# Kernel tuning notes

Measured on AMD Instinct MI355X. Metric: run time of the kernel, lower is better.

Reference implementation:

```python
import jax, jax.numpy as jnp
import numpy as np

B, T, C = 2, 2048, 2048
NH, NKV, HD = 16, 4, 128
GATE_CH = 12
WINDOW = 1024


def apply_rotary_emb(x, cos, sin):
    # x: (B,T,H,HD); cos/sin: (1,T,1,HD//2)
    d = x.shape[3] // 2
    x1, x2 = x[..., :d], x[..., d:]
    return jnp.concatenate([x1 * cos + x2 * sin, -x1 * sin + x2 * cos], axis=3)


def rms_norm(x):
    return x * jax.lax.rsqrt(jnp.mean(jnp.square(x), axis=-1, keepdims=True) + 1e-06)


def setup_inputs() -> dict:
    key = jax.random.key(0)
    ks = jax.random.split(key, 7)
    # realistic RoPE tables
    theta = 10000.0 ** (-jnp.arange(HD // 2, dtype=jnp.float32) / (HD // 2))
    ang = jnp.arange(T, dtype=jnp.float32)[:, None] * theta[None, :]
    cos = jnp.cos(ang)[None, :, None, :]
    sin = jnp.sin(ang)[None, :, None, :]
    return {
        "x": jax.random.normal(ks[0], (B, T, C), jnp.float32),
        "ve": jax.random.normal(ks[1], (B, T, NKV * HD), jnp.float32),
        "cos": cos,
        "sin": sin,
        "Wq": 0.02 * jax.random.normal(ks[2], (NH * HD, C), jnp.float32),
        "Wk": 0.02 * jax.random.normal(ks[3], (NKV * HD, C), jnp.float32),
        "Wv": 0.02 * jax.random.normal(ks[4], (NKV * HD, C), jnp.float32),
        "Wproj": 0.02 * jax.random.normal(ks[5], (C, C), jnp.float32),
        "Wgate": 0.02 * jax.random.normal(ks[6], (NKV, GATE_CH), jnp.float32),
        "window_size": WINDOW,
    }


def reference(x, ve, cos, sin, Wq, Wk, Wv, Wproj, Wgate, window_size):
    B_, T_, C_ = x.shape
    q = (x @ Wq.T).reshape(B_, T_, NH, HD)
    k = (x @ Wk.T).reshape(B_, T_, NKV, HD)
    v = (x @ Wv.T).reshape(B_, T_, NKV, HD)
    # value-embedding gate-add
    gate = 3.0 * jax.nn.sigmoid(x[..., :GATE_CH] @ Wgate.T)  # (B,T,NKV)
    v = v + gate[..., None] * ve.reshape(B_, T_, NKV, HD)
    # RoPE + QK RMSNorm + scale
    q = rms_norm(apply_rotary_emb(q, cos, sin)) * 1.2
    k = rms_norm(apply_rotary_emb(k, cos, sin)) * 1.2
    # GQA head-repeat
    rep = NH // NKV
    k = jnp.repeat(k, rep, axis=2)
    v = jnp.repeat(v, rep, axis=2)
    # sliding-window causal bias (window_size > 0 branch)
    r = jnp.arange(T_)
    mask = (r[None, :] <= r[:, None]) & (r[:, None] - r[None, :] <= window_size)
    bias = jnp.where(mask, 0.0, jnp.finfo(x.dtype).min)  # (T,T)
    scores = jnp.einsum("bthd,bshd->bhts", q, k) * (1.0 / np.sqrt(HD).astype(np.float32))
    scores = scores + bias[None, None, :, :]
    w = jax.nn.softmax(scores, axis=-1)
    y = jnp.einsum("bhts,bshd->bthd", w, v).reshape(B_, T_, -1)
    return y @ Wproj.T
```

## Files before the change

kernel.cpp:

```cpp
#include <hip/hip_runtime.h>
#include <hip/hip_bf16.h>

#define BB   2
#define TT   2048
#define CC   2048
#define NHq  16
#define NKVq 4
#define HDq  128
#define ROWS (BB*TT)
#define NQKV (NHq*HDq + 2*NKVq*HDq)

using bf16 = __hip_bfloat16;
using short8  = __attribute__((ext_vector_type(8))) short;
using short4v = __attribute__((ext_vector_type(4))) short;
using f32x4   = __attribute__((ext_vector_type(4))) float;

#define MFMA16(a,b,c) __builtin_amdgcn_mfma_f32_16x16x32_bf16((a),(b),(c),0,0,0)

__device__ __forceinline__ void gll16(const bf16* g, void* l) {
    __builtin_amdgcn_global_load_lds((const __attribute__((address_space(1))) void*)g,
                                     (__attribute__((address_space(3))) void*)l,
                                     16, 0, 0);
}

__global__ void cast_all(const float* __restrict__ x,  const float* __restrict__ wq,
                         const float* __restrict__ wk, const float* __restrict__ wv,
                         const float* __restrict__ wp, bf16* __restrict__ dst) {
    long e = ((long)blockIdx.x * 256 + threadIdx.x) * 4;
    const float* src; long off;
    if (e < 8388608L)       { src = x;  off = e; }
    else if (e < 12582912L) { src = wq; off = e - 8388608L; }
    else if (e < 13631488L) { src = wk; off = e - 12582912L; }
    else if (e < 14680064L) { src = wv; off = e - 13631488L; }
    else                    { src = wp; off = e - 14680064L; }
    float4 v = *reinterpret_cast<const float4*>(src + off);
    ushort4 o;
    o.x = __bfloat16_as_ushort(__float2bfloat16(v.x));
    o.y = __bfloat16_as_ushort(__float2bfloat16(v.y));
    o.z = __bfloat16_as_ushort(__float2bfloat16(v.z));
    o.w = __bfloat16_as_ushort(__float2bfloat16(v.w));
    *reinterpret_cast<ushort4*>(dst + e) = o;
}

template<int OUT_F32>
__global__ __launch_bounds__(256) void gemm_bt(const bf16* __restrict__ A,
                                               const bf16* __restrict__ B,
                                               void* __restrict__ Cp,
                                               int M, int N, int K) {
    const int bm = blockIdx.x * 128;
    const int bn = blockIdx.y * 128;
    const int tid = threadIdx.x;
    const int lane = tid & 63;
    const int w = tid >> 6;
    const int wr = w >> 1, wc = w & 1;

    __shared__ __align__(16) bf16 As[128 * 64];
    __shared__ __align__(16) bf16 Bs[128 * 64];

    f32x4 acc[4][4];
#pragma unroll
    for (int i = 0; i < 4; ++i)
#pragma unroll
        for (int j = 0; j < 4; ++j) acc[i][j] = f32x4{0.f, 0.f, 0.f, 0.f};

    const int srow = tid >> 3;
    const int sch  = tid & 7;

    const int fr = lane & 15;
    const int kq = lane >> 4;

    for (int k0 = 0; k0 < K; k0 += 64) {
        __syncthreads();
#pragma unroll
        for (int i = 0; i < 4; ++i) {
            int row = i * 32 + srow;
            int c = sch ^ (row & 7);
            gll16(&A[(size_t)(bm + row) * K + k0 + c * 8], (char*)As + i * 4096 + tid * 16);
            gll16(&B[(size_t)(bn + row) * K + k0 + c * 8], (char*)Bs + i * 4096 + tid * 16);
        }
        __syncthreads();

#pragma unroll
        for (int kk = 0; kk < 2; ++kk) {
            short8 af[4], bfr[4];
#pragma unroll
            for (int m = 0; m < 4; ++m) {
                int r = wr * 64 + m * 16 + fr;
                af[m] = *reinterpret_cast<const short8*>(
                    (const char*)As + r * 128 + (((kk * 4 + kq) ^ (r & 7)) * 16));
            }
#pragma unroll
            for (int n = 0; n < 4; ++n) {
                int r = wc * 64 + n * 16 + fr;
                bfr[n] = *reinterpret_cast<const short8*>(
                    (const char*)Bs + r * 128 + (((kk * 4 + kq) ^ (r & 7)) * 16));
            }
            __builtin_amdgcn_s_setprio(1);
#pragma unroll
            for (int m = 0; m < 4; ++m)
#pragma unroll
                for (int n = 0; n < 4; ++n)
                    acc[m][n] = MFMA16(af[m], bfr[n], acc[m][n]);
            __builtin_amdgcn_s_setprio(0);
        }
    }

    const int cr = (lane >> 4) * 4;
    const int cc = lane & 15;
#pragma unroll
    for (int m = 0; m < 4; ++m)
#pragma unroll
        for (int n = 0; n < 4; ++n) {
            int row = bm + wr * 64 + m * 16 + cr;
            int col = bn + wc * 64 + n * 16 + cc;
#pragma unroll
            for (int j = 0; j < 4; ++j) {
                float v = acc[m][n][j];
                if (OUT_F32) ((float*)Cp)[(size_t)(row + j) * N + col] = v;
                else         ((bf16*)Cp)[(size_t)(row + j) * N + col] = __float2bfloat16(v);
            }
        }
}

__global__ __launch_bounds__(256) void postproc(const float* __restrict__ x,
                                                const float* __restrict__ ve,
                                                const float* __restrict__ cosb,
                                                const float* __restrict__ sinb,
                                                const float* __restrict__ Wgate,
                                                bf16* __restrict__ qkv) {
    const int row = blockIdx.x;
    const int t = row & (TT - 1);
    const int tid = threadIdx.x;
    __shared__ float gate_s[NKVq];
    if (tid < NKVq) {
        float g = 0.f;
#pragma unroll
        for (int c = 0; c < 12; ++c) g += x[(size_t)row * CC + c] * Wgate[tid * 12 + c];
        gate_s[tid] = 3.0f / (1.0f + __expf(-g));
    }
    __syncthreads();

    bf16* qkvr = qkv + (size_t)row * NQKV;

#pragma unroll
    for (int i = 0; i < 2; ++i) {
        int idx = tid + i * 256;
        float v = __bfloat162float(qkvr[2560 + idx]);
        v += gate_s[idx >> 7] * ve[(size_t)row * 512 + idx];
        qkvr[2560 + idx] = __float2bfloat16(v);
    }

    const int lane = tid & 63;
    const int w = tid >> 6;
    const float cv = cosb[(size_t)t * 64 + lane];
    const float sv = sinb[(size_t)t * 64 + lane];
    for (int hh = w; hh < NHq + NKVq; hh += 4) {
        int off = (hh < NHq) ? hh * HDq : 2048 + (hh - NHq) * HDq;
        float x1 = __bfloat162float(qkvr[off + lane]);
        float x2 = __bfloat162float(qkvr[off + 64 + lane]);
        float r1 =  x1 * cv + x2 * sv;
        float r2 = -x1 * sv + x2 * cv;
        float ss = r1 * r1 + r2 * r2;
#pragma unroll
        for (int m = 1; m < 64; m <<= 1) ss += __shfl_xor(ss, m);
        float sc = rsqrtf(ss * (1.0f / 128.0f) + 1e-6f) * 1.2f;
        qkvr[off + lane]      = __float2bfloat16(r1 * sc);
        qkvr[off + 64 + lane] = __float2bfloat16(r2 * sc);
    }
}

__global__ __launch_bounds__(256, 2) void attn_mfma(const bf16* __restrict__ qkv,
                                                    bf16* __restrict__ y,
                                                    const int* __restrict__ winp) {
    const int bid = blockIdx.x;
    const int group = bid >> 8, idx = bid & 255;
    const int bh = idx >> 3, jj = idx & 7;
    const int qt = group ? jj : (15 - jj);
    const int h = bh & 15, b = bh >> 4;
    const int t0 = qt * 128;
    const int kvh = h >> 2;
    const int tid = threadIdx.x;
    const int lane = tid & 63;
    const int w = tid >> 6;
    const int window = winp[0];

    __shared__ __align__(16) bf16 Ks[2][64 * 128];
    __shared__ __align__(16) bf16 Vt[2][128 * 64];
    __shared__ __align__(16) bf16 Ps[4][32 * 64];

    const int fr = lane & 15;
    const int kq = (lane >> 4) * 8;
    const int hi = lane >> 4;
    const float scl2 = 0.08838834764831845f * 1.4426950408889634f;
    const float CAP = 24.0f;

    short8 qf[2][4];
#pragma unroll
    for (int mi = 0; mi < 2; ++mi) {
        const bf16* qp = qkv + ((size_t)(b * TT) + t0 + w * 32 + mi * 16 + fr) * NQKV + h * HDq;
#pragma unroll
        for (int c = 0; c < 4; ++c) {
            short8 v = *reinterpret_cast<const short8*>(&qp[c * 32 + kq]);
#pragma unroll
            for (int e = 0; e < 8; ++e) {
                float f = __bfloat162float(__ushort_as_bfloat16((ushort)v[e])) * scl2;
                v[e] = (short)__bfloat16_as_ushort(__float2bfloat16(f));
            }
            qf[mi][c] = v;
        }
    }

    f32x4 acc[2][8];
#pragma unroll
    for (int mi = 0; mi < 2; ++mi)
#pragma unroll
        for (int n = 0; n < 8; ++n) acc[mi][n] = f32x4{0.f, 0.f, 0.f, 0.f};
    float lrow[2][4];
#pragma unroll
    for (int mi = 0; mi < 2; ++mi)
#pragma unroll
        for (int j = 0; j < 4; ++j) lrow[mi][j] = 0.f;

    int s_lo = t0 - window; if (s_lo < 0) s_lo = 0; s_lo &= ~63;
    const int s_end = t0 + 128;

    const bf16* Kg = qkv + (size_t)b * TT * NQKV + 2048 + kvh * HDq;
    const bf16* Vg = Kg + 512;

    const int str = tid >> 4;
    const int sti = tid & 15;
    const int vf  = tid & 15;
    const int vdc = (tid >> 4) * 8;

    short8 vr[4];

#pragma unroll
    for (int p = 0; p < 4; ++p) {
        int row = p * 16 + str;
        int c16 = sti ^ (row & 7);
        gll16(&Kg[(size_t)(s_lo + row) * NQKV + c16 * 8], (char*)Ks[0] + p * 4096 + tid * 16);
    }
#pragma unroll
    for (int i = 0; i < 4; ++i)
        vr[i] = *reinterpret_cast<const short8*>(&Vg[(size_t)(s_lo + 16 * i + vf) * NQKV + vdc]);
#pragma unroll
    for (int j = 0; j < 8; ++j) {
        short4v col;
        col[0] = vr[0][j]; col[1] = vr[1][j]; col[2] = vr[2][j]; col[3] = vr[3][j];
        *reinterpret_cast<short4v*>((char*)Vt[0] + (vdc + j) * 128 + ((8 * vf) ^ (j << 4))) = col;
    }
    __syncthreads();

    int cur = 0;
    for (int sk = s_lo; sk < s_end; sk += 64) {
        const bool hn = (sk + 64 < s_end);

        if (hn) {
#pragma unroll
            for (int p = 0; p < 4; ++p) {
                int row = p * 16 + str;
                int c16 = sti ^ (row & 7);
                gll16(&Kg[(size_t)(sk + 64 + row) * NQKV + c16 * 8],
                      (char*)Ks[cur ^ 1] + p * 4096 + tid * 16);
            }
#pragma unroll
            for (int i = 0; i < 4; ++i)
                vr[i] = *reinterpret_cast<const short8*>(&Vg[(size_t)(sk + 64 + 16 * i + vf) * NQKV + vdc]);
        }

        f32x4 S[2][4];
#pragma unroll
        for (int mi = 0; mi < 2; ++mi)
#pragma unroll
            for (int n = 0; n < 4; ++n) S[mi][n] = f32x4{0.f, 0.f, 0.f, 0.f};
        __builtin_amdgcn_s_setprio(1);
#pragma unroll
        for (int n = 0; n < 4; ++n) {
            int rb = n * 16 + fr;
#pragma unroll
            for (int c = 0; c < 4; ++c) {
                int colb = c * 64 + kq * 2;
                short8 kf = *reinterpret_cast<const short8*>(
                    (const char*)Ks[cur] + rb * 256 + (colb ^ ((rb & 7) << 4)));
                S[0][n] = MFMA16(qf[0][c], kf, S[0][n]);
                S[1][n] = MFMA16(qf[1][c], kf, S[1][n]);
            }
        }
        __builtin_amdgcn_s_setprio(0);

        const int rw0 = t0 + w * 32;
        const bool interior = (sk + 63 <= rw0) && (rw0 + 31 - sk <= window);
#pragma unroll
        for (int mi = 0; mi < 2; ++mi) {
#pragma unroll
            for (int j = 0; j < 4; ++j) {
                const int rl = hi * 4 + j;
                float s0, s1, s2, s3;
                if (interior) {
                    s0 = S[mi][0][j]; s1 = S[mi][1][j];
                    s2 = S[mi][2][j]; s3 = S[mi][3][j];
                } else {
                    const int r = rw0 + mi * 16 + rl;
                    int c0 = sk + fr, c1 = c0 + 16, c2 = c0 + 32, c3 = c0 + 48;
                    s0 = (c0 <= r && r - c0 <= window) ? S[mi][0][j] : -1e30f;
                    s1 = (c1 <= r && r - c1 <= window) ? S[mi][1][j] : -1e30f;
                    s2 = (c2 <= r && r - c2 <= window) ? S[mi][2][j] : -1e30f;
                    s3 = (c3 <= r && r - c3 <= window) ? S[mi][3][j] : -1e30f;
                }
                float p0 = exp2f(s0 - CAP);
                float p1 = exp2f(s1 - CAP);
                float p2 = exp2f(s2 - CAP);
                float p3 = exp2f(s3 - CAP);
                lrow[mi][j] += (p0 + p1) + (p2 + p3);
                short4v pk;
                pk[0] = (short)__bfloat16_as_ushort(__float2bfloat16(p0));
                pk[1] = (short)__bfloat16_as_ushort(__float2bfloat16(p1));
                pk[2] = (short)__bfloat16_as_ushort(__float2bfloat16(p2));
                pk[3] = (short)__bfloat16_as_ushort(__float2bfloat16(p3));
                const int prow = mi * 16 + rl;
                *reinterpret_cast<short4v*>(
                    (char*)Ps + w * 4096 + prow * 128 + ((8 * fr) ^ ((prow & 7) << 4))) = pk;
            }
        }

        if (hn) {
#pragma unroll
            for (int j = 0; j < 8; ++j) {
                short4v col;
                col[0] = vr[0][j]; col[1] = vr[1][j]; col[2] = vr[2][j]; col[3] = vr[3][j];
                *reinterpret_cast<short4v*>((char*)Vt[cur ^ 1] + (vdc + j) * 128 + ((8 * vf) ^ (j << 4))) = col;
            }
        }

        __builtin_amdgcn_s_setprio(1);
#pragma unroll
        for (int c2 = 0; c2 < 2; ++c2) {
            short8 pa0 = *reinterpret_cast<const short8*>(
                (char*)Ps + w * 4096 + fr * 128 + ((c2 * 64 + hi * 16) ^ ((fr & 7) << 4)));
            short8 pa1 = *reinterpret_cast<const short8*>(
                (char*)Ps + w * 4096 + (16 + fr) * 128 + ((c2 * 64 + hi * 16) ^ ((fr & 7) << 4)));
#pragma unroll
            for (int n = 0; n < 8; ++n) {
                short8 vb = *reinterpret_cast<const short8*>(
                    (char*)Vt[cur] + (n * 16 + fr) * 128 + ((c2 * 64 + hi * 16) ^ ((fr & 7) << 4)));
                acc[0][n] = MFMA16(pa0, vb, acc[0][n]);
                acc[1][n] = MFMA16(pa1, vb, acc[1][n]);
            }
        }
        __builtin_amdgcn_s_setprio(0);

        __syncthreads();
        cur ^= 1;
    }

#pragma unroll
    for (int mi = 0; mi < 2; ++mi)
#pragma unroll
        for (int j = 0; j < 4; ++j) {
            float l = lrow[mi][j];
#pragma unroll
            for (int mm = 1; mm < 16; mm <<= 1) l += __shfl_xor(l, mm);
            const int r = t0 + w * 32 + mi * 16 + hi * 4 + j;
            float inv = 1.f / l;
            bf16* yr = y + ((size_t)(b * TT) + r) * CC + h * HDq;
#pragma unroll
            for (int n = 0; n < 8; ++n)
                yr[n * 16 + fr] = __float2bfloat16(acc[mi][n][j] * inv);
        }
}

extern "C" void kernel_launch(void* const* d_in, const int* in_sizes, int n_in,
                              void* d_out, int out_size, void* d_ws, size_t ws_size,
                              hipStream_t stream) {
    const float* x     = (const float*)d_in[0];
    const float* ve    = (const float*)d_in[1];
    const float* cosb  = (const float*)d_in[2];
    const float* sinb  = (const float*)d_in[3];
    const float* Wq    = (const float*)d_in[4];
    const float* Wk    = (const float*)d_in[5];
    const float* Wv    = (const float*)d_in[6];
    const float* Wproj = (const float*)d_in[7];
    const float* Wgate = (const float*)d_in[8];
    const int*   winp  = (const int*)d_in[9];

    bf16* xb     = (bf16*)d_ws;
    bf16* wqkvb  = xb + (size_t)ROWS * CC;
    bf16* wprojb = wqkvb + (size_t)NQKV * CC;
    bf16* qkvb   = wprojb + (size_t)CC * CC;
    bf16* yb     = xb;

    cast_all<<<18432, 256, 0, stream>>>(x, Wq, Wk, Wv, Wproj, xb);

    gemm_bt<0><<<dim3(ROWS / 128, NQKV / 128), 256, 0, stream>>>(xb, wqkvb, qkvb, ROWS, NQKV, CC);

    postproc<<<ROWS, 256, 0, stream>>>(x, ve, cosb, sinb, Wgate, qkvb);

    attn_mfma<<<BB * NHq * (TT / 128), 256, 0, stream>>>(qkvb, yb, winp);

    gemm_bt<1><<<dim3(ROWS / 128, CC / 128), 256, 0, stream>>>(yb, wprojb, d_out, ROWS, CC, CC);
}
```

Baseline: 178.4 us.

## Split attention query tile across 8 waves and specialize K/V loader waves

The attention kernel now runs 512 threads (8 waves) per 128-row query tile, each wave owning 16 query rows instead of 32. That halves the per-wave accumulator and score registers. K staging moves to waves 4-7 and the V transpose to waves 0-3, so each load path is handled by dedicated waves. This aims to raise wave-level parallelism and latency hiding. The cost is that each K/V fragment read from LDS is reused across fewer rows, which means more LDS traffic per MFMA, and the barrier now has to sync twice as many waves.

```diff
diff --git a/kernel.cpp b/kernel.cpp
--- a/kernel.cpp
+++ b/kernel.cpp
@@ -169,7 +169,7 @@
     }
 }
 
-__global__ __launch_bounds__(256, 2) void attn_mfma(const bf16* __restrict__ qkv,
+__global__ __launch_bounds__(512, 2) void attn_mfma(const bf16* __restrict__ qkv,
                                                     bf16* __restrict__ y,
                                                     const int* __restrict__ winp) {
     const int bid = blockIdx.x;
@@ -186,7 +186,7 @@
 
     __shared__ __align__(16) bf16 Ks[2][64 * 128];
     __shared__ __align__(16) bf16 Vt[2][128 * 64];
-    __shared__ __align__(16) bf16 Ps[4][32 * 64];
+    __shared__ __align__(16) bf16 Ps[8][16 * 64];
 
     const int fr = lane & 15;
     const int kq = (lane >> 4) * 8;
@@ -194,10 +194,9 @@
     const float scl2 = 0.08838834764831845f * 1.4426950408889634f;
     const float CAP = 24.0f;
 
-    short8 qf[2][4];
-#pragma unroll
-    for (int mi = 0; mi < 2; ++mi) {
-        const bf16* qp = qkv + ((size_t)(b * TT) + t0 + w * 32 + mi * 16 + fr) * NQKV + h * HDq;
+    short8 qf[4];
+    {
+        const bf16* qp = qkv + ((size_t)(b * TT) + t0 + w * 16 + fr) * NQKV + h * HDq;
 #pragma unroll
         for (int c = 0; c < 4; ++c) {
             short8 v = *reinterpret_cast<const short8*>(&qp[c * 32 + kq]);
@@ -206,20 +205,14 @@
                 float f = __bfloat162float(__ushort_as_bfloat16((ushort)v[e])) * scl2;
                 v[e] = (short)__bfloat16_as_ushort(__float2bfloat16(f));
             }
-            qf[mi][c] = v;
-        }
-    }
-
-    f32x4 acc[2][8];
-#pragma unroll
-    for (int mi = 0; mi < 2; ++mi)
-#pragma unroll
-        for (int n = 0; n < 8; ++n) acc[mi][n] = f32x4{0.f, 0.f, 0.f, 0.f};
-    float lrow[2][4];
-#pragma unroll
-    for (int mi = 0; mi < 2; ++mi)
-#pragma unroll
-        for (int j = 0; j < 4; ++j) lrow[mi][j] = 0.f;
+            qf[c] = v;
+        }
+    }
+
+    f32x4 acc[8];
+#pragma unroll
+    for (int n = 0; n < 8; ++n) acc[n] = f32x4{0.f, 0.f, 0.f, 0.f};
+    float lrow[4] = {0.f, 0.f, 0.f, 0.f};
 
     int s_lo = t0 - window; if (s_lo < 0) s_lo = 0; s_lo &= ~63;
     const int s_end = t0 + 128;
@@ -227,27 +220,32 @@
     const bf16* Kg = qkv + (size_t)b * TT * NQKV + 2048 + kvh * HDq;
     const bf16* Vg = Kg + 512;
 
-    const int str = tid >> 4;
-    const int sti = tid & 15;
+    const bool isv = (w < 4);
     const int vf  = tid & 15;
-    const int vdc = (tid >> 4) * 8;
+    const int vdc = ((tid >> 4) & 15) * 8;
+    const int ktid = tid & 255;
+    const int str = ktid >> 4;
+    const int sti = ktid & 15;
 
     short8 vr[4];
 
-#pragma unroll
-    for (int p = 0; p < 4; ++p) {
-        int row = p * 16 + str;
-        int c16 = sti ^ (row & 7);
-        gll16(&Kg[(size_t)(s_lo + row) * NQKV + c16 * 8], (char*)Ks[0] + p * 4096 + tid * 16);
-    }
-#pragma unroll
-    for (int i = 0; i < 4; ++i)
-        vr[i] = *reinterpret_cast<const short8*>(&Vg[(size_t)(s_lo + 16 * i + vf) * NQKV + vdc]);
-#pragma unroll
-    for (int j = 0; j < 8; ++j) {
-        short4v col;
-        col[0] = vr[0][j]; col[1] = vr[1][j]; col[2] = vr[2][j]; col[3] = vr[3][j];
-        *reinterpret_cast<short4v*>((char*)Vt[0] + (vdc + j) * 128 + ((8 * vf) ^ (j << 4))) = col;
+    if (!isv) {
+#pragma unroll
+        for (int p = 0; p < 4; ++p) {
+            int row = p * 16 + str;
+            int c16 = sti ^ (row & 7);
+            gll16(&Kg[(size_t)(s_lo + row) * NQKV + c16 * 8], (char*)Ks[0] + p * 4096 + ktid * 16);
+        }
+    } else {
+#pragma unroll
+        for (int i = 0; i < 4; ++i)
+            vr[i] = *reinterpret_cast<const short8*>(&Vg[(size_t)(s_lo + 16 * i + vf) * NQKV + vdc]);
+#pragma unroll
+        for (int j = 0; j < 8; ++j) {
+            short4v col;
+            col[0] = vr[0][j]; col[1] = vr[1][j]; col[2] = vr[2][j]; col[3] = vr[3][j];
+            *reinterpret_cast<short4v*>((char*)Vt[0] + (vdc + j) * 128 + ((8 * vf) ^ (j << 4))) = col;
+        }
     }
     __syncthreads();
 
@@ -256,23 +254,24 @@
         const bool hn = (sk + 64 < s_end);
 
         if (hn) {
-#pragma unroll
-            for (int p = 0; p < 4; ++p) {
-                int row = p * 16 + str;
-                int c16 = sti ^ (row & 7);
-                gll16(&Kg[(size_t)(sk + 64 + row) * NQKV + c16 * 8],
-                      (char*)Ks[cur ^ 1] + p * 4096 + tid * 16);
-            }
-#pragma unroll
-            for (int i = 0; i < 4; ++i)
-                vr[i] = *reinterpret_cast<const short8*>(&Vg[(size_t)(sk + 64 + 16 * i + vf) * NQKV + vdc]);
-        }
-
-        f32x4 S[2][4];
-#pragma unroll
-        for (int mi = 0; mi < 2; ++mi)
-#pragma unroll
-            for (int n = 0; n < 4; ++n) S[mi][n] = f32x4{0.f, 0.f, 0.f, 0.f};
+            if (!isv) {
+#pragma unroll
+                for (int p = 0; p < 4; ++p) {
+                    int row = p * 16 + str;
+                    int c16 = sti ^ (row & 7);
+                    gll16(&Kg[(size_t)(sk + 64 + row) * NQKV + c16 * 8],
+                          (char*)Ks[cur ^ 1] + p * 4096 + ktid * 16);
+                }
+            } else {
+#pragma unroll
+                for (int i = 0; i < 4; ++i)
+                    vr[i] = *reinterpret_cast<const short8*>(&Vg[(size_t)(sk + 64 + 16 * i + vf) * NQKV + vdc]);
+            }
+        }
+
+        f32x4 S[4];
+#pragma unroll
+        for (int n = 0; n < 4; ++n) S[n] = f32x4{0.f, 0.f, 0.f, 0.f};
         __builtin_amdgcn_s_setprio(1);
 #pragma unroll
         for (int n = 0; n < 4; ++n) {
@@ -282,48 +281,42 @@
                 int colb = c * 64 + kq * 2;
                 short8 kf = *reinterpret_cast<const short8*>(
                     (const char*)Ks[cur] + rb * 256 + (colb ^ ((rb & 7) << 4)));
-                S[0][n] = MFMA16(qf[0][c], kf, S[0][n]);
-                S[1][n] = MFMA16(qf[1][c], kf, S[1][n]);
+                S[n] = MFMA16(qf[c], kf, S[n]);
             }
         }
         __builtin_amdgcn_s_setprio(0);
 
-        const int rw0 = t0 + w * 32;
-        const bool interior = (sk + 63 <= rw0) && (rw0 + 31 - sk <= window);
-#pragma unroll
-        for (int mi = 0; mi < 2; ++mi) {
-#pragma unroll
-            for (int j = 0; j < 4; ++j) {
-                const int rl = hi * 4 + j;
-                float s0, s1, s2, s3;
-                if (interior) {
-                    s0 = S[mi][0][j]; s1 = S[mi][1][j];
-                    s2 = S[mi][2][j]; s3 = S[mi][3][j];
-                } else {
-                    const int r = rw0 + mi * 16 + rl;
-                    int c0 = sk + fr, c1 = c0 + 16, c2 = c0 + 32, c3 = c0 + 48;
-                    s0 = (c0 <= r && r - c0 <= window) ? S[mi][0][j] : -1e30f;
-                    s1 = (c1 <= r && r - c1 <= window) ? S[mi][1][j] : -1e30f;
-                    s2 = (c2 <= r && r - c2 <= window) ? S[mi][2][j] : -1e30f;
-                    s3 = (c3 <= r && r - c3 <= window) ? S[mi][3][j] : -1e30f;
-                }
-                float p0 = exp2f(s0 - CAP);
-                float p1 = exp2f(s1 - CAP);
-                float p2 = exp2f(s2 - CAP);
-                float p3 = exp2f(s3 - CAP);
-                lrow[mi][j] += (p0 + p1) + (p2 + p3);
-                short4v pk;
-                pk[0] = (short)__bfloat16_as_ushort(__float2bfloat16(p0));
-                pk[1] = (short)__bfloat16_as_ushort(__float2bfloat16(p1));
-                pk[2] = (short)__bfloat16_as_ushort(__float2bfloat16(p2));
-                pk[3] = (short)__bfloat16_as_ushort(__float2bfloat16(p3));
-                const int prow = mi * 16 + rl;
-                *reinterpret_cast<short4v*>(
-                    (char*)Ps + w * 4096 + prow * 128 + ((8 * fr) ^ ((prow & 7) << 4))) = pk;
-            }
-        }
-
-        if (hn) {
+        const int rw0 = t0 + w * 16;
+        const bool interior = (sk + 63 <= rw0) && (rw0 + 15 - sk <= window);
+#pragma unroll
+        for (int j = 0; j < 4; ++j) {
+            const int rl = hi * 4 + j;
+            float s0, s1, s2, s3;
+            if (interior) {
+                s0 = S[0][j]; s1 = S[1][j]; s2 = S[2][j]; s3 = S[3][j];
+            } else {
+                const int r = rw0 + rl;
+                int c0 = sk + fr, c1 = c0 + 16, c2 = c0 + 32, c3 = c0 + 48;
+                s0 = (c0 <= r && r - c0 <= window) ? S[0][j] : -1e30f;
+                s1 = (c1 <= r && r - c1 <= window) ? S[1][j] : -1e30f;
+                s2 = (c2 <= r && r - c2 <= window) ? S[2][j] : -1e30f;
+                s3 = (c3 <= r && r - c3 <= window) ? S[3][j] : -1e30f;
+            }
+            float p0 = exp2f(s0 - CAP);
+            float p1 = exp2f(s1 - CAP);
+            float p2 = exp2f(s2 - CAP);
+            float p3 = exp2f(s3 - CAP);
+            lrow[j] += (p0 + p1) + (p2 + p3);
+            short4v pk;
+            pk[0] = (short)__bfloat16_as_ushort(__float2bfloat16(p0));
+            pk[1] = (short)__bfloat16_as_ushort(__float2bfloat16(p1));
+            pk[2] = (short)__bfloat16_as_ushort(__float2bfloat16(p2));
+            pk[3] = (short)__bfloat16_as_ushort(__float2bfloat16(p3));
+            *reinterpret_cast<short4v*>(
+                (char*)Ps + w * 2048 + rl * 128 + ((8 * fr) ^ ((rl & 7) << 4))) = pk;
+        }
+
+        if (hn && isv) {
 #pragma unroll
             for (int j = 0; j < 8; ++j) {
                 short4v col;
@@ -335,16 +328,13 @@
         __builtin_amdgcn_s_setprio(1);
 #pragma unroll
         for (int c2 = 0; c2 < 2; ++c2) {
-            short8 pa0 = *reinterpret_cast<const short8*>(
-                (char*)Ps + w * 4096 + fr * 128 + ((c2 * 64 + hi * 16) ^ ((fr & 7) << 4)));
-            short8 pa1 = *reinterpret_cast<const short8*>(
-                (char*)Ps + w * 4096 + (16 + fr) * 128 + ((c2 * 64 + hi * 16) ^ ((fr & 7) << 4)));
+            short8 pa = *reinterpret_cast<const short8*>(
+                (char*)Ps + w * 2048 + fr * 128 + ((c2 * 64 + hi * 16) ^ ((fr & 7) << 4)));
 #pragma unroll
             for (int n = 0; n < 8; ++n) {
                 short8 vb = *reinterpret_cast<const short8*>(
                     (char*)Vt[cur] + (n * 16 + fr) * 128 + ((c2 * 64 + hi * 16) ^ ((fr & 7) << 4)));
-                acc[0][n] = MFMA16(pa0, vb, acc[0][n]);
-                acc[1][n] = MFMA16(pa1, vb, acc[1][n]);
+                acc[n] = MFMA16(pa, vb, acc[n]);
             }
         }
         __builtin_amdgcn_s_setprio(0);
@@ -354,19 +344,17 @@
     }
 
 #pragma unroll
-    for (int mi = 0; mi < 2; ++mi)
-#pragma unroll
-        for (int j = 0; j < 4; ++j) {
-            float l = lrow[mi][j];
-#pragma unroll
-            for (int mm = 1; mm < 16; mm <<= 1) l += __shfl_xor(l, mm);
-            const int r = t0 + w * 32 + mi * 16 + hi * 4 + j;
-            float inv = 1.f / l;
-            bf16* yr = y + ((size_t)(b * TT) + r) * CC + h * HDq;
-#pragma unroll
-            for (int n = 0; n < 8; ++n)
-                yr[n * 16 + fr] = __float2bfloat16(acc[mi][n][j] * inv);
-        }
+    for (int j = 0; j < 4; ++j) {
+        float l = lrow[j];
+#pragma unroll
+        for (int mm = 1; mm < 16; mm <<= 1) l += __shfl_xor(l, mm);
+        const int r = t0 + w * 16 + hi * 4 + j;
+        float inv = 1.f / l;
+        bf16* yr = y + ((size_t)(b * TT) + r) * CC + h * HDq;
+#pragma unroll
+        for (int n = 0; n < 8; ++n)
+            yr[n * 16 + fr] = __float2bfloat16(acc[n][j] * inv);
+    }
 }
 
 extern "C" void kernel_launch(void* const* d_in, const int* in_sizes, int n_in,
@@ -395,7 +383,7 @@
 
     postproc<<<ROWS, 256, 0, stream>>>(x, ve, cosb, sinb, Wgate, qkvb);
 
-    attn_mfma<<<BB * NHq * (TT / 128), 256, 0, stream>>>(qkvb, yb, winp);
+    attn_mfma<<<BB * NHq * (TT / 128), 512, 0, stream>>>(qkvb, yb, winp);
 
     gemm_bt<1><<<dim3(ROWS / 128, CC / 128), 256, 0, stream>>>(yb, wprojb, d_out, ROWS, CC, CC);
 }
```

Measured after the change: 192.5 us. 7.9% more time.
